# Kernel optimization log

Measured on AMD Instinct MI355X. Metric: run time of the kernel, lower is better.

## Reference

```python
import jax, jax.numpy as jnp
import numpy as np

N = 131072
E = 128   # component_dim
H = 4     # num heads
Dh = E // H
OUT = 768 # embedding_dim

def setup_inputs() -> dict:
    key = jax.random.key(0)
    ks = jax.random.split(key, 20)
    inp = {
        'device_ids': jax.random.randint(ks[0], (N,), 0, 10),
        'pseudo_ids': jax.random.randint(ks[1], (N,), 0, 10),
        'attr_ids':   jax.random.randint(ks[2], (N,), 0, 100),
        'unit_ids':   jax.random.randint(ks[3], (N,), 0, 20),
        'values':     jax.random.normal(ks[4], (N,), dtype=jnp.float32),
        'mask':       jax.random.randint(ks[5], (N, 5), 0, 2, dtype=jnp.int32),
        # embedding tables (std=0.02 per _initialize_embeddings)
        'dev_table':    0.02 * jax.random.normal(ks[6], (10, E), dtype=jnp.float32),
        'pseudo_table': 0.02 * jax.random.normal(ks[7], (10, E), dtype=jnp.float32),
        'attr_table':   0.02 * jax.random.normal(ks[8], (100, E), dtype=jnp.float32),
        'unit_table':   0.02 * jax.random.normal(ks[9], (20, E), dtype=jnp.float32),
        # value_projection: Linear(1, E)
        'val_w': jax.random.normal(ks[10], (E, 1), dtype=jnp.float32) * (6.0 / (1 + E)) ** 0.5,
        'val_b': jnp.zeros((E,), dtype=jnp.float32),
        # MultiheadAttention packed qkv + out proj
        'in_proj_w':  jax.random.normal(ks[11], (3 * E, E), dtype=jnp.float32) / np.sqrt(E),
        'in_proj_b':  jnp.zeros((3 * E,), dtype=jnp.float32),
        'out_proj_w': jax.random.normal(ks[12], (E, E), dtype=jnp.float32) / np.sqrt(E),
        'out_proj_b': jnp.zeros((E,), dtype=jnp.float32),
        # output_projection: Linear(E, OUT)
        'out_w': jax.random.normal(ks[13], (OUT, E), dtype=jnp.float32) * (6.0 / (E + OUT)) ** 0.5,
        'out_b': jnp.zeros((OUT,), dtype=jnp.float32),
    }
    return inp

def reference(device_ids, pseudo_ids, attr_ids, unit_ids, values, mask,
              dev_table, pseudo_table, attr_table, unit_table,
              val_w, val_b, in_proj_w, in_proj_b, out_proj_w, out_proj_b,
              out_w, out_b):
    # gather the 4 embedding tables + value projection -> [N, 5, E]
    d = dev_table[device_ids]
    p = pseudo_table[pseudo_ids]
    a = attr_table[attr_ids]
    v = values[:, None] * val_w[:, 0][None, :] + val_b  # Linear(1, E)
    u = unit_table[unit_ids]
    comp = jnp.stack([d, p, a, v, u], axis=1)
    comp = comp * mask[..., None].astype(comp.dtype)  # missing components -> zeros
    # 5-token MHA (batch_first, packed qkv)
    qkv = comp @ in_proj_w.T + in_proj_b              # [N, 5, 3E]
    q, k, vv = jnp.split(qkv, 3, axis=-1)
    q = q.reshape(-1, 5, H, Dh)
    k = k.reshape(-1, 5, H, Dh)
    vv = vv.reshape(-1, 5, H, Dh)
    scores = jnp.einsum('nqhd,nkhd->nhqk', q, k) / np.sqrt(Dh)
    attn = jax.nn.softmax(scores, axis=-1)
    o = jnp.einsum('nhqk,nkhd->nqhd', attn, vv).reshape(-1, 5, E)
    o = o @ out_proj_w.T + out_proj_b                  # [N, 5, E]
    composed = jnp.mean(o, axis=1)                     # [N, E]
    return composed @ out_w.T + out_b                  # [N, OUT]
```

## Files before the change

kernel.cpp:

```cpp
#include <hip/hip_runtime.h>


typedef __attribute__((ext_vector_type(8))) short bf16x8;
typedef __attribute__((ext_vector_type(4))) float floatx4;

__device__ __forceinline__ unsigned short f32_bf16(float f) {
  unsigned int x = __float_as_uint(f);
  x += 0x7FFFu + ((x >> 16) & 1u);
  return (unsigned short)(x >> 16);
}

__global__ void k_proj_tables(const float* __restrict__ dev_t, const float* __restrict__ pse_t,
                              const float* __restrict__ att_t, const float* __restrict__ unt_t,
                              const float* __restrict__ val_w, const float* __restrict__ val_b,
                              const float* __restrict__ W ,
                              float* __restrict__ out ) {
  __shared__ float src[128];
  int r = blockIdx.x;
  const float* s;
  if (r < 10)        s = dev_t + r * 128;
  else if (r < 20)   s = pse_t + (r - 10) * 128;
  else if (r < 120)  s = att_t + (r - 20) * 128;
  else if (r < 140)  s = unt_t + (r - 120) * 128;
  else if (r == 140) s = val_w;
  else               s = val_b;
  int t = threadIdx.x;
  if (t < 128) src[t] = s[t];
  __syncthreads();
  const float* wr = W + t * 128;
  float acc = 0.f;
#pragma unroll 8
  for (int e = 0; e < 128; ++e) acc = fmaf(wr[e], src[e], acc);
  out[r * 384 + t] = acc;
}

__global__ void k_fuse_w2(const float* __restrict__ out_w ,
                          const float* __restrict__ opw ,
                          const float* __restrict__ opb ,
                          const float* __restrict__ out_b ,
                          unsigned short* __restrict__ W2 ,
                          float* __restrict__ b2 ) {
  __shared__ float row[128];
  __shared__ float red[128];
  int r = blockIdx.x, c = threadIdx.x;
  row[c] = out_w[r * 128 + c];
  __syncthreads();
  float acc = 0.f;
#pragma unroll 8
  for (int k = 0; k < 128; ++k) acc = fmaf(row[k], opw[k * 128 + c], acc);
  W2[r * 128 + c] = f32_bf16(acc);
  red[c] = row[c] * opb[c];
  __syncthreads();
#pragma unroll
  for (int s = 64; s > 0; s >>= 1) {
    if (c < s) red[c] += red[c + s];
    __syncthreads();
  }
  if (c == 0) b2[r] = red[0] + out_b[r];
}


#define LDS_STRIDE 136

__device__ __forceinline__ void load8f(float d[8], const float* __restrict__ p, int c) {
  float4 a = *(const float4*)(p + c);
  float4 b = *(const float4*)(p + c + 4);
  d[0] = a.x; d[1] = a.y; d[2] = a.z; d[3] = a.w;
  d[4] = b.x; d[5] = b.y; d[6] = b.z; d[7] = b.w;
}

__global__ __launch_bounds__(256, 2)
void k_main(const int* __restrict__ dev_ids, const int* __restrict__ pse_ids,
            const int* __restrict__ att_ids, const int* __restrict__ unt_ids,
            const float* __restrict__ values, const int* __restrict__ mask,
            const float* __restrict__ proj ,
            const float* __restrict__ bias ,
            const unsigned short* __restrict__ W2 ,
            const float* __restrict__ b2 ,
            float* __restrict__ out ) {
  __shared__ __align__(16) unsigned short sMean[64 * LDS_STRIDE];

  const int tid = threadIdx.x;
  const int lr = tid >> 2;
  const int h  = tid & 3;
  const int n  = blockIdx.x * 64 + lr;

  {
    const float* p[5];
    p[0] = proj + (size_t)dev_ids[n] * 384;
    p[1] = proj + (size_t)(10 + pse_ids[n]) * 384;
    p[2] = proj + (size_t)(20 + att_ids[n]) * 384;
    p[3] = proj + (size_t)140 * 384;
    p[4] = proj + (size_t)(120 + unt_ids[n]) * 384;
    const float* pvb = proj + (size_t)141 * 384;
    const float val = values[n];
    float m[5];
#pragma unroll
    for (int t = 0; t < 5; ++t) m[t] = (float)mask[n * 5 + t];

    float s[25];
#pragma unroll
    for (int i = 0; i < 25; ++i) s[i] = 0.f;

#pragma unroll
    for (int dc = 0; dc < 4; ++dc) {
      const int qc = h * 32 + dc * 8;
      const int kc = qc + 128;
      float bq[8], bk[8];
      load8f(bq, bias, qc);
      load8f(bk, bias, kc);
      float qv[5][8], kv[5][8];
#pragma unroll
      for (int t = 0; t < 5; ++t) {
        float rq[8], rk[8];
        if (t == 3) {
          float aq[8], ab[8];
          load8f(aq, p[3], qc); load8f(ab, pvb, qc);
#pragma unroll
          for (int j = 0; j < 8; ++j) rq[j] = fmaf(val, aq[j], ab[j]);
          load8f(aq, p[3], kc); load8f(ab, pvb, kc);
#pragma unroll
          for (int j = 0; j < 8; ++j) rk[j] = fmaf(val, aq[j], ab[j]);
        } else {
          load8f(rq, p[t], qc);
          load8f(rk, p[t], kc);
        }
#pragma unroll
        for (int j = 0; j < 8; ++j) {
          qv[t][j] = fmaf(m[t], rq[j], bq[j]);
          kv[t][j] = fmaf(m[t], rk[j], bk[j]);
        }
      }
#pragma unroll
      for (int qt = 0; qt < 5; ++qt)
#pragma unroll
        for (int kt = 0; kt < 5; ++kt) {
          float acc = s[qt * 5 + kt];
#pragma unroll
          for (int j = 0; j < 8; ++j) acc = fmaf(qv[qt][j], kv[kt][j], acc);
          s[qt * 5 + kt] = acc;
        }
    }

    const float scale = 0.17677669529663687f;
    float w5[5] = {0.f, 0.f, 0.f, 0.f, 0.f};
#pragma unroll
    for (int qt = 0; qt < 5; ++qt) {
      const float* r = s + qt * 5;
      float mx = fmaxf(fmaxf(fmaxf(r[0], r[1]), fmaxf(r[2], r[3])), r[4]);
      float e[5], l = 0.f;
#pragma unroll
      for (int kt = 0; kt < 5; ++kt) { e[kt] = __expf((r[kt] - mx) * scale); l += e[kt]; }
      const float inv = 0.2f / l;
#pragma unroll
      for (int kt = 0; kt < 5; ++kt) w5[kt] = fmaf(e[kt], inv, w5[kt]);
    }
    const float sumw = w5[0] + w5[1] + w5[2] + w5[3] + w5[4];

#pragma unroll
    for (int dc = 0; dc < 4; ++dc) {
      const int vc = 256 + h * 32 + dc * 8;
      float bv[8];
      load8f(bv, bias, vc);
      float acc[8];
#pragma unroll
      for (int j = 0; j < 8; ++j) acc[j] = sumw * bv[j];
#pragma unroll
      for (int kt = 0; kt < 5; ++kt) {
        float rv[8];
        if (kt == 3) {
          float av[8], ab[8];
          load8f(av, p[3], vc); load8f(ab, pvb, vc);
#pragma unroll
          for (int j = 0; j < 8; ++j) rv[j] = fmaf(val, av[j], ab[j]);
        } else {
          load8f(rv, p[kt], vc);
        }
        const float cw = w5[kt] * m[kt];
#pragma unroll
        for (int j = 0; j < 8; ++j) acc[j] = fmaf(cw, rv[j], acc[j]);
      }
      uint4 pk;
      pk.x = (unsigned)f32_bf16(acc[0]) | ((unsigned)f32_bf16(acc[1]) << 16);
      pk.y = (unsigned)f32_bf16(acc[2]) | ((unsigned)f32_bf16(acc[3]) << 16);
      pk.z = (unsigned)f32_bf16(acc[4]) | ((unsigned)f32_bf16(acc[5]) << 16);
      pk.w = (unsigned)f32_bf16(acc[6]) | ((unsigned)f32_bf16(acc[7]) << 16);
      *(uint4*)((char*)sMean + (size_t)lr * (LDS_STRIDE * 2) + h * 64 + dc * 16) = pk;
    }
  }
  __syncthreads();

  {
    const int w    = tid >> 6;
    const int lane = tid & 63;
    const int ln16 = lane & 15;
    const int lq   = lane >> 4;

    bf16x8 afrag[4][4];
#pragma unroll
    for (int mt = 0; mt < 4; ++mt)
#pragma unroll
      for (int ks = 0; ks < 4; ++ks)
        afrag[mt][ks] = *(const bf16x8*)((const char*)sMean +
                          (size_t)(mt * 16 + ln16) * (LDS_STRIDE * 2) + ks * 64 + lq * 16);

    const int rowbase = blockIdx.x * 64;
#pragma unroll 2
    for (int nt = 0; nt < 12; ++nt) {
      const int col = w * 192 + nt * 16 + ln16;
      const unsigned short* bp = W2 + (size_t)col * 128 + lq * 8;
      bf16x8 bfrag[4];
#pragma unroll
      for (int ks = 0; ks < 4; ++ks)
        bfrag[ks] = *(const bf16x8*)(bp + ks * 32);

      floatx4 acc[4];
#pragma unroll
      for (int mt = 0; mt < 4; ++mt) acc[mt] = (floatx4){0.f, 0.f, 0.f, 0.f};
#pragma unroll
      for (int ks = 0; ks < 4; ++ks)
#pragma unroll
        for (int mt = 0; mt < 4; ++mt)
          acc[mt] = __builtin_amdgcn_mfma_f32_16x16x32_bf16(afrag[mt][ks], bfrag[ks], acc[mt], 0, 0, 0);

      const float bb = b2[col];
#pragma unroll
      for (int mt = 0; mt < 4; ++mt) {
        const int r0 = rowbase + mt * 16 + lq * 4;
#pragma unroll
        for (int r = 0; r < 4; ++r)
          out[(size_t)(r0 + r) * 768 + col] = acc[mt][r] + bb;
      }
    }
  }
}

extern "C" void kernel_launch(void* const* d_in, const int* in_sizes, int n_in,
                              void* d_out, int out_size, void* d_ws, size_t ws_size,
                              hipStream_t stream) {
  const int*   dev_ids = (const int*)d_in[0];
  const int*   pse_ids = (const int*)d_in[1];
  const int*   att_ids = (const int*)d_in[2];
  const int*   unt_ids = (const int*)d_in[3];
  const float* values  = (const float*)d_in[4];
  const int*   mask    = (const int*)d_in[5];
  const float* dev_t   = (const float*)d_in[6];
  const float* pse_t   = (const float*)d_in[7];
  const float* att_t   = (const float*)d_in[8];
  const float* unt_t   = (const float*)d_in[9];
  const float* val_w   = (const float*)d_in[10];
  const float* val_b   = (const float*)d_in[11];
  const float* ipw     = (const float*)d_in[12];
  const float* ipb     = (const float*)d_in[13];
  const float* opw     = (const float*)d_in[14];
  const float* opb     = (const float*)d_in[15];
  const float* out_w   = (const float*)d_in[16];
  const float* out_b   = (const float*)d_in[17];
  float* out = (float*)d_out;

  const int N = in_sizes[0];

  float* proj = (float*)d_ws;
  float* b2   = proj + 142 * 384;
  unsigned short* W2 = (unsigned short*)(b2 + 768);

  k_proj_tables<<<142, 384, 0, stream>>>(dev_t, pse_t, att_t, unt_t, val_w, val_b, ipw, proj);
  k_fuse_w2<<<768, 128, 0, stream>>>(out_w, opw, opb, out_b, W2, b2);
  k_main<<<N / 64, 256, 0, stream>>>(dev_ids, pse_ids, att_ids, unt_ids, values, mask,
                                     proj, ipb, W2, b2, out);
  (void)out_size; (void)ws_size; (void)n_in;
}
```

Before: 593.2 us.

## Precompute per-head QK dot products between table rows and gather scores

```diff
diff --git a/kernel.cpp b/kernel.cpp
--- a/kernel.cpp
+++ b/kernel.cpp
@@ -59,22 +59,65 @@
   if (c == 0) b2[r] = red[0] + out_b[r];
 }
 
+__global__ void k_dots(const float* __restrict__ proj, const float* __restrict__ bias,
+                       float* __restrict__ D, float* __restrict__ E,
+                       float* __restrict__ F, float* __restrict__ G,
+                       unsigned short* __restrict__ PvB) {
+  __shared__ float qs[128];
+  const int q = blockIdx.x;
+  const int t = threadIdx.x;
+  if (t < 128) qs[t] = proj[q * 384 + t];
+  __syncthreads();
+  for (int o = t; o < 568; o += 256) {
+    const int k = o >> 2, h = o & 3;
+    const float* kp = proj + k * 384 + 128 + h * 32;
+    const float* qp = qs + h * 32;
+    float acc = 0.f;
+#pragma unroll
+    for (int d = 0; d < 32; ++d) acc = fmaf(qp[d], kp[d], acc);
+    D[(size_t)(q * 142 + k) * 4 + h] = acc;
+  }
+  if (t < 4) {
+    const int h = t;
+    float e = 0.f, f = 0.f;
+#pragma unroll
+    for (int d = 0; d < 32; ++d) {
+      e = fmaf(qs[h * 32 + d], bias[128 + h * 32 + d], e);
+      f = fmaf(bias[h * 32 + d], proj[q * 384 + 128 + h * 32 + d], f);
+    }
+    E[q * 4 + h] = e;
+    F[q * 4 + h] = f;
+    if (q == 0) {
+      float g = 0.f;
+#pragma unroll
+      for (int d = 0; d < 32; ++d) g = fmaf(bias[h * 32 + d], bias[128 + h * 32 + d], g);
+      G[h] = g;
+    }
+  }
+  if (t >= 128) {
+    const int x = t - 128;
+    const int h = x >> 5, dc = (x >> 3) & 3, j = x & 7;
+    PvB[q * 128 + dc * 32 + h * 8 + j] = f32_bf16(proj[q * 384 + 256 + x]);
+    if (q == 0) PvB[142 * 128 + dc * 32 + h * 8 + j] = f32_bf16(bias[256 + x]);
+  }
+}
 
 #define LDS_STRIDE 136
 
-__device__ __forceinline__ void load8f(float d[8], const float* __restrict__ p, int c) {
-  float4 a = *(const float4*)(p + c);
-  float4 b = *(const float4*)(p + c + 4);
-  d[0] = a.x; d[1] = a.y; d[2] = a.z; d[3] = a.w;
-  d[4] = b.x; d[5] = b.y; d[6] = b.z; d[7] = b.w;
+__device__ __forceinline__ void unpack8(float d[8], uint4 p) {
+  d[0] = __uint_as_float(p.x << 16); d[1] = __uint_as_float(p.x & 0xffff0000u);
+  d[2] = __uint_as_float(p.y << 16); d[3] = __uint_as_float(p.y & 0xffff0000u);
+  d[4] = __uint_as_float(p.z << 16); d[5] = __uint_as_float(p.z & 0xffff0000u);
+  d[6] = __uint_as_float(p.w << 16); d[7] = __uint_as_float(p.w & 0xffff0000u);
 }
 
 __global__ __launch_bounds__(256, 2)
 void k_main(const int* __restrict__ dev_ids, const int* __restrict__ pse_ids,
             const int* __restrict__ att_ids, const int* __restrict__ unt_ids,
             const float* __restrict__ values, const int* __restrict__ mask,
-            const float* __restrict__ proj ,
-            const float* __restrict__ bias ,
+            const float* __restrict__ D, const float* __restrict__ E,
+            const float* __restrict__ F, const float* __restrict__ G,
+            const unsigned short* __restrict__ PvB,
             const unsigned short* __restrict__ W2 ,
             const float* __restrict__ b2 ,
             float* __restrict__ out ) {
@@ -86,61 +129,56 @@
   const int n  = blockIdx.x * 64 + lr;
 
   {
-    const float* p[5];
-    p[0] = proj + (size_t)dev_ids[n] * 384;
-    p[1] = proj + (size_t)(10 + pse_ids[n]) * 384;
-    p[2] = proj + (size_t)(20 + att_ids[n]) * 384;
-    p[3] = proj + (size_t)140 * 384;
-    p[4] = proj + (size_t)(120 + unt_ids[n]) * 384;
-    const float* pvb = proj + (size_t)141 * 384;
+    int R[4];
+    R[0] = dev_ids[n];
+    R[1] = 10 + pse_ids[n];
+    R[2] = 20 + att_ids[n];
+    R[3] = 120 + unt_ids[n];
     const float val = values[n];
     float m[5];
 #pragma unroll
     for (int t = 0; t < 5; ++t) m[t] = (float)mask[n * 5 + t];
-
+    const float mi[4] = {m[0], m[1], m[2], m[4]};
+
+    float Dqk[4][4], Dw_k[4], Db_k[4], Dq_w[4], Dq_b[4], Eq[4], Fk[4];
+#pragma unroll
+    for (int i = 0; i < 4; ++i) {
+#pragma unroll
+      for (int j = 0; j < 4; ++j)
+        Dqk[i][j] = D[(size_t)(R[i] * 142 + R[j]) * 4 + h];
+      Dw_k[i] = D[(size_t)(140 * 142 + R[i]) * 4 + h];
+      Db_k[i] = D[(size_t)(141 * 142 + R[i]) * 4 + h];
+      Dq_w[i] = D[(size_t)(R[i] * 142 + 140) * 4 + h];
+      Dq_b[i] = D[(size_t)(R[i] * 142 + 141) * 4 + h];
+      Eq[i]   = E[R[i] * 4 + h];
+      Fk[i]   = F[R[i] * 4 + h];
+    }
+    const float Dww = D[(size_t)(140 * 142 + 140) * 4 + h];
+    const float Dwb = D[(size_t)(140 * 142 + 141) * 4 + h];
+    const float Dbw = D[(size_t)(141 * 142 + 140) * 4 + h];
+    const float Dbb = D[(size_t)(141 * 142 + 141) * 4 + h];
+    const float Ew = E[140 * 4 + h], Eb = E[141 * 4 + h];
+    const float Fw = F[140 * 4 + h], Fb = F[141 * 4 + h];
+    const float Gh = G[h];
+
+    const float E3  = val * Ew + Eb;
+    const float F3  = val * Fw + Fb;
+    const float D33 = val * val * Dww + val * (Dwb + Dbw) + Dbb;
+
+    const int ti[4] = {0, 1, 2, 4};
     float s[25];
 #pragma unroll
-    for (int i = 0; i < 25; ++i) s[i] = 0.f;
-
-#pragma unroll
-    for (int dc = 0; dc < 4; ++dc) {
-      const int qc = h * 32 + dc * 8;
-      const int kc = qc + 128;
-      float bq[8], bk[8];
-      load8f(bq, bias, qc);
-      load8f(bk, bias, kc);
-      float qv[5][8], kv[5][8];
-#pragma unroll
-      for (int t = 0; t < 5; ++t) {
-        float rq[8], rk[8];
-        if (t == 3) {
-          float aq[8], ab[8];
-          load8f(aq, p[3], qc); load8f(ab, pvb, qc);
-#pragma unroll
-          for (int j = 0; j < 8; ++j) rq[j] = fmaf(val, aq[j], ab[j]);
-          load8f(aq, p[3], kc); load8f(ab, pvb, kc);
-#pragma unroll
-          for (int j = 0; j < 8; ++j) rk[j] = fmaf(val, aq[j], ab[j]);
-        } else {
-          load8f(rq, p[t], qc);
-          load8f(rk, p[t], kc);
-        }
-#pragma unroll
-        for (int j = 0; j < 8; ++j) {
-          qv[t][j] = fmaf(m[t], rq[j], bq[j]);
-          kv[t][j] = fmaf(m[t], rk[j], bk[j]);
-        }
-      }
-#pragma unroll
-      for (int qt = 0; qt < 5; ++qt)
-#pragma unroll
-        for (int kt = 0; kt < 5; ++kt) {
-          float acc = s[qt * 5 + kt];
-#pragma unroll
-          for (int j = 0; j < 8; ++j) acc = fmaf(qv[qt][j], kv[kt][j], acc);
-          s[qt * 5 + kt] = acc;
-        }
-    }
+    for (int i = 0; i < 4; ++i)
+#pragma unroll
+      for (int j = 0; j < 4; ++j)
+        s[ti[i] * 5 + ti[j]] = mi[i] * (mi[j] * Dqk[i][j] + Eq[i]) + mi[j] * Fk[j] + Gh;
+#pragma unroll
+    for (int j = 0; j < 4; ++j)
+      s[3 * 5 + ti[j]] = m[3] * (mi[j] * (val * Dw_k[j] + Db_k[j]) + E3) + mi[j] * Fk[j] + Gh;
+#pragma unroll
+    for (int i = 0; i < 4; ++i)
+      s[ti[i] * 5 + 3] = mi[i] * (m[3] * (val * Dq_w[i] + Dq_b[i]) + Eq[i]) + m[3] * F3 + Gh;
+    s[3 * 5 + 3] = m[3] * (m[3] * D33 + E3) + m[3] * F3 + Gh;
 
     const float scale = 0.17677669529663687f;
     float w5[5] = {0.f, 0.f, 0.f, 0.f, 0.f};
@@ -157,28 +195,19 @@
     }
     const float sumw = w5[0] + w5[1] + w5[2] + w5[3] + w5[4];
 
+    const int   vr[7] = {R[0], R[1], R[2], R[3], 140, 141, 142};
+    const float vc[7] = {w5[0] * m[0], w5[1] * m[1], w5[2] * m[2], w5[4] * m[4],
+                         w5[3] * m[3] * val, w5[3] * m[3], sumw};
 #pragma unroll
     for (int dc = 0; dc < 4; ++dc) {
-      const int vc = 256 + h * 32 + dc * 8;
-      float bv[8];
-      load8f(bv, bias, vc);
-      float acc[8];
-#pragma unroll
-      for (int j = 0; j < 8; ++j) acc[j] = sumw * bv[j];
-#pragma unroll
-      for (int kt = 0; kt < 5; ++kt) {
-        float rv[8];
-        if (kt == 3) {
-          float av[8], ab[8];
-          load8f(av, p[3], vc); load8f(ab, pvb, vc);
-#pragma unroll
-          for (int j = 0; j < 8; ++j) rv[j] = fmaf(val, av[j], ab[j]);
-        } else {
-          load8f(rv, p[kt], vc);
-        }
-        const float cw = w5[kt] * m[kt];
-#pragma unroll
-        for (int j = 0; j < 8; ++j) acc[j] = fmaf(cw, rv[j], acc[j]);
+      float acc[8] = {0.f, 0.f, 0.f, 0.f, 0.f, 0.f, 0.f, 0.f};
+#pragma unroll
+      for (int p = 0; p < 7; ++p) {
+        uint4 pk = *(const uint4*)(PvB + (size_t)vr[p] * 128 + dc * 32 + h * 8);
+        float v[8];
+        unpack8(v, pk);
+#pragma unroll
+        for (int j = 0; j < 8; ++j) acc[j] = fmaf(vc[p], v[j], acc[j]);
       }
       uint4 pk;
       pk.x = (unsigned)f32_bf16(acc[0]) | ((unsigned)f32_bf16(acc[1]) << 16);
@@ -261,12 +290,18 @@
   const int N = in_sizes[0];
 
   float* proj = (float*)d_ws;
-  float* b2   = proj + 142 * 384;
+  float* b2   = proj + 54528;
   unsigned short* W2 = (unsigned short*)(b2 + 768);
+  float* D = (float*)(W2 + 768 * 128);
+  float* E = D + 142 * 142 * 4;
+  float* F = E + 142 * 4;
+  float* G = F + 142 * 4;
+  unsigned short* PvB = (unsigned short*)(G + 4);
 
   k_proj_tables<<<142, 384, 0, stream>>>(dev_t, pse_t, att_t, unt_t, val_w, val_b, ipw, proj);
   k_fuse_w2<<<768, 128, 0, stream>>>(out_w, opw, opb, out_b, W2, b2);
+  k_dots<<<142, 256, 0, stream>>>(proj, ipb, D, E, F, G, PvB);
   k_main<<<N / 64, 256, 0, stream>>>(dev_ids, pse_ids, att_ids, unt_ids, values, mask,
-                                     proj, ipb, W2, b2, out);
+                                     D, E, F, G, PvB, W2, b2, out);
   (void)out_size; (void)ws_size; (void)n_in;
 }
```

Result: faster. 490.1 us (-17.4%).
